# Optimization experiments

Hardware: AMD Instinct MI355X
Metric: run time of the kernel (lower is better)

The kernel has to match this reference:

```python
import jax, jax.numpy as jnp
import numpy as np

L = 16384   # nodes (rows)
E = 131072  # edges
SP = 20000  # column positions (nodes + periodic images)
C = 512     # embed_dim
H = 8       # heads
DH = C // H # head dim = 64
HID = 1024  # ffn hidden


def setup_inputs() -> dict:
    key = jax.random.key(0)
    ks = jax.random.split(key, 16)
    p = lambda k, shape: jax.random.normal(k, shape, dtype=jnp.float32) * 0.02
    return dict(
        x=jax.random.normal(ks[0], (L, C), dtype=jnp.float32),
        row_index=jax.random.randint(ks[1], (E,), 0, L),
        col_index=jax.random.randint(ks[2], (E,), 0, L),
        to_col_index=jax.random.randint(ks[3], (E,), 0, SP),
        att_bias=jax.random.normal(ks[4], (E, H), dtype=jnp.float32),
        pos_att_bias=jax.random.normal(ks[5], (E, H), dtype=jnp.float32),
        dist=jax.random.uniform(ks[6], (E,), minval=0.5, maxval=5.0),
        pos=jax.random.normal(ks[7], (L, 3), dtype=jnp.float32),
        col_pos=jax.random.normal(ks[8], (SP, 3), dtype=jnp.float32),
        ln1_g=jnp.ones((C,), jnp.float32), ln1_b=jnp.zeros((C,), jnp.float32),
        ln2_g=jnp.ones((C,), jnp.float32), ln2_b=jnp.zeros((C,), jnp.float32),
        Wq=p(ks[9], (C, C)), bq=jnp.zeros((C,), jnp.float32),
        Wk=p(ks[10], (C, C)), bk=jnp.zeros((C,), jnp.float32),
        Wv=p(ks[11], (C, C)), bv=jnp.zeros((C,), jnp.float32),
        Wvec=p(ks[12], (3, C)), bvec=jnp.zeros((C,), jnp.float32),
        Wo=p(ks[13], (C, C)), bo=jnp.zeros((C,), jnp.float32),
        W1=p(ks[14], (C, HID)), b1=jnp.zeros((HID,), jnp.float32),
        W2=p(ks[15], (HID, C)), b2=jnp.zeros((C,), jnp.float32),
    )


def _ln(x, g, b, eps=1e-5):
    mu = jnp.mean(x, -1, keepdims=True)
    v = jnp.mean((x - mu) ** 2, -1, keepdims=True)
    return (x - mu) * jax.lax.rsqrt(v + eps) * g + b


def reference(x, row_index, col_index, to_col_index, att_bias, pos_att_bias,
              dist, pos, col_pos, ln1_g, ln1_b, ln2_g, ln2_b,
              Wq, bq, Wk, bk, Wv, bv, Wvec, bvec, Wo, bo, W1, b1, W2, b2):
    Lx = x.shape[0]
    # --- pre-norm + Euclidean sparse attention ---
    z = _ln(x, ln1_g, ln1_b)
    q = (z @ Wq + bq).reshape(Lx, H, DH)
    k = (z @ Wk + bk).reshape(Lx, H, DH)
    v = (z @ Wv + bv).reshape(Lx, H, DH)
    qe = q[row_index]          # (E,H,DH) gather
    ke = k[col_index]          # (E,H,DH)
    ve = v[col_index]          # (E,H,DH)
    # relative unit direction from receiving node to (PBC-shifted) column node
    rel = (col_pos[to_col_index] - pos[row_index]) / dist[:, None]   # (E,3)
    ve = ve + (rel @ Wvec + bvec).reshape(-1, H, DH)
    # Euclidean (negative squared L2) attention score + positional bias
    score = -jnp.sum((qe - ke) ** 2, axis=-1) / np.float32(np.sqrt(DH)) + pos_att_bias  # (E,H)
    # segment softmax over edges grouped by row_index
    m = jax.ops.segment_max(score, row_index, num_segments=Lx)       # (L,H)
    m = jnp.where(jnp.isfinite(m), m, 0.0)
    pexp = jnp.exp(score - m[row_index])
    den = jax.ops.segment_sum(pexp, row_index, num_segments=Lx)      # (L,H)
    deng = den[row_index]
    alpha = pexp / jnp.where(deng == 0.0, 1.0, deng)                 # (E,H)
    out = jax.ops.segment_sum(alpha[:, :, None] * ve, row_index, num_segments=Lx)
    att = out.reshape(Lx, C) @ Wo + bo
    x = x + att
    # --- pre-norm + feed-forward ---
    z2 = _ln(x, ln2_g, ln2_b)
    ff = jax.nn.gelu(z2 @ W1 + b1) @ W2 + b2
    return x + ff
```

## Files before the change

### kernel.cpp

```cpp
#include <hip/hip_runtime.h>

#define L_NODES 16384
#define E_EDGES 131072
#define CDIM 512
#define QKVDIM 1536
#define HEADS 8
#define DHEAD 64
#define HID 1024

typedef __attribute__((ext_vector_type(8))) short bf16x8;
typedef __attribute__((ext_vector_type(4))) float f32x4;

__device__ inline unsigned short f2b(float f) {
    union { float f; unsigned int u; } v{f};
    unsigned int r = (v.u + 0x7fffu + ((v.u >> 16) & 1u)) >> 16;
    return (unsigned short)r;
}
__device__ inline float b2f(unsigned short h) {
    union { unsigned int u; float f; } v;
    v.u = (unsigned int)h << 16;
    return v.f;
}

__device__ inline void async_lds16(const void* g, void* l) {
    __builtin_amdgcn_global_load_lds(
        (const __attribute__((address_space(1))) unsigned int*)g,
        (__attribute__((address_space(3))) unsigned int*)l,
        16, 0, 0);
}

__global__ __launch_bounds__(256) void ln_bf16_kernel(
    const float* __restrict__ x, const float* __restrict__ g,
    const float* __restrict__ b, short* __restrict__ out)
{
    int row = blockIdx.x;
    int t = threadIdx.x;
    const float2* xr = (const float2*)(x + (size_t)row * CDIM);
    float2 v = xr[t];
    float s = v.x + v.y;
    float sq = v.x * v.x + v.y * v.y;
    for (int off = 32; off; off >>= 1) {
        s += __shfl_xor(s, off);
        sq += __shfl_xor(sq, off);
    }
    __shared__ float ss[4], sqs[4];
    int wave = t >> 6, lane = t & 63;
    if (lane == 0) { ss[wave] = s; sqs[wave] = sq; }
    __syncthreads();
    s = ss[0] + ss[1] + ss[2] + ss[3];
    sq = sqs[0] + sqs[1] + sqs[2] + sqs[3];
    float mu = s * (1.0f / CDIM);
    float var = sq * (1.0f / CDIM) - mu * mu;
    float inv = rsqrtf(var + 1e-5f);
    int c = t * 2;
    unsigned short h0 = f2b((v.x - mu) * inv * g[c] + b[c]);
    unsigned short h1 = f2b((v.y - mu) * inv * g[c + 1] + b[c + 1]);
    unsigned int packed = ((unsigned int)h1 << 16) | h0;
    *(unsigned int*)(out + (size_t)row * CDIM + c) = packed;
}

__global__ void transpose_bf16_kernel(const float* __restrict__ W, short* __restrict__ WT,
                                      int K, int N)
{
    __shared__ float tile[32][33];
    int n0 = blockIdx.x * 32, k0 = blockIdx.y * 32;
    int tx = threadIdx.x, ty = threadIdx.y;
    for (int r = 0; r < 4; r++) {
        int k = ty + r * 8;
        tile[k][tx] = W[(size_t)(k0 + k) * N + n0 + tx];
    }
    __syncthreads();
    for (int r = 0; r < 4; r++) {
        int n = ty + r * 8;
        WT[(size_t)(n0 + n) * K + k0 + tx] = f2b(tile[tx][n]);
    }
}

__global__ void pack_bias_kernel(const float* __restrict__ bq, const float* __restrict__ bk,
                                 const float* __restrict__ bv, float* __restrict__ out)
{
    int i = blockIdx.x * 256 + threadIdx.x;
    if (i < CDIM) out[i] = bq[i];
    else if (i < 2 * CDIM) out[i] = bk[i - CDIM];
    else out[i] = bv[i - 2 * CDIM];
}

__global__ __launch_bounds__(256) void gemm_bf16_kernel(
    const short* __restrict__ A, const short* __restrict__ B,
    const float* __restrict__ bias, const float* __restrict__ res,
    float* __restrict__ outf, short* __restrict__ outb,
    int M, int N, int K, int act)
{
    __shared__ short As[128 * 32];
    __shared__ short Bs[128 * 32];
    int t = threadIdx.x;
    int bm = blockIdx.y * 128, bn = blockIdx.x * 128;
    int wave = t >> 6, lane = t & 63;
    int wm = (wave & 1) * 64, wn = (wave >> 1) * 64;
    int crow = lane & 15, quad = lane >> 4;

    f32x4 acc[4][4] = {};

    for (int k0 = 0; k0 < K; k0 += 32) {
#pragma unroll
        for (int c = 0; c < 2; c++) {
            int idx = c * 256 + t;
            int row = idx >> 2, chunk = idx & 3;
            async_lds16(A + (size_t)(bm + row) * K + k0 + chunk * 8,
                        (char*)As + c * 4096 + wave * 1024 + lane * 16);
            async_lds16(B + (size_t)(bn + row) * K + k0 + chunk * 8,
                        (char*)Bs + c * 4096 + wave * 1024 + lane * 16);
        }
        __syncthreads();
        bf16x8 af[4], bg[4];
#pragma unroll
        for (int i = 0; i < 4; i++)
            af[i] = *(const bf16x8*)&As[(wm + i * 16 + crow) * 32 + quad * 8];
#pragma unroll
        for (int j = 0; j < 4; j++)
            bg[j] = *(const bf16x8*)&Bs[(wn + j * 16 + crow) * 32 + quad * 8];
#pragma unroll
        for (int i = 0; i < 4; i++)
#pragma unroll
            for (int j = 0; j < 4; j++)
                acc[i][j] = __builtin_amdgcn_mfma_f32_16x16x32_bf16(af[i], bg[j], acc[i][j], 0, 0, 0);
        __syncthreads();
    }

#pragma unroll
    for (int i = 0; i < 4; i++) {
#pragma unroll
        for (int j = 0; j < 4; j++) {
            int n = bn + wn + j * 16 + crow;
            float bi = bias ? bias[n] : 0.0f;
#pragma unroll
            for (int r = 0; r < 4; r++) {
                int mrow = bm + wm + i * 16 + quad * 4 + r;
                float val = acc[i][j][r] + bi;
                if (act) {
                    float u = 0.7978845608028654f * (val + 0.044715f * val * val * val);
                    val = 0.5f * val * (1.0f + tanhf(u));
                }
                if (res) val += res[(size_t)mrow * N + n];
                if (outf) outf[(size_t)mrow * N + n] = val;
                if (outb) outb[(size_t)mrow * N + n] = f2b(val);
            }
        }
    }
}

__global__ void hist_kernel(const int* __restrict__ row_index, int* __restrict__ cnt)
{
    int e = blockIdx.x * 256 + threadIdx.x;
    if (e < E_EDGES) atomicAdd(&cnt[row_index[e]], 1);
}

__global__ void scan_kernel(const int* __restrict__ cnt, int* __restrict__ row_start,
                            int* __restrict__ cursor)
{
    int t = threadIdx.x;
    const int PER = L_NODES / 64;
    int local = 0;
    for (int i = 0; i < PER; i++) local += cnt[t * PER + i];
    int v = local;
    for (int off = 1; off < 64; off <<= 1) {
        int u = __shfl_up(v, off);
        if (t >= off) v += u;
    }
    int run = v - local;
    for (int i = 0; i < PER; i++) {
        row_start[t * PER + i] = run;
        cursor[t * PER + i] = run;
        run += cnt[t * PER + i];
    }
    if (t == 63) row_start[L_NODES] = run;
}

__global__ void scatter_kernel(const int* __restrict__ row_index, const int* __restrict__ col_index,
                               const int* __restrict__ to_col_index, const float* __restrict__ dist,
                               int* __restrict__ cursor, int4* __restrict__ epack)
{
    int e = blockIdx.x * 256 + threadIdx.x;
    if (e < E_EDGES) {
        int p = atomicAdd(&cursor[row_index[e]], 1);
        epack[p] = make_int4(col_index[e], to_col_index[e], __float_as_int(dist[e]), e);
    }
}

__global__ __launch_bounds__(512) void attn_kernel(
    const short* __restrict__ qkv,
    const int4* __restrict__ epack,
    const float* __restrict__ pos_att_bias,
    const float* __restrict__ pos, const float* __restrict__ col_pos,
    const float* __restrict__ Wvec, const float* __restrict__ bvec,
    const int* __restrict__ row_start,
    short* __restrict__ out_bf)
{
    int r = blockIdx.x;
    int t = threadIdx.x;
    int h = t >> 6;
    int c = t;
    float qv = b2f(((const unsigned short*)qkv)[(size_t)r * QKVDIM + c]);
    float wv0 = Wvec[c], wv1 = Wvec[CDIM + c], wv2 = Wvec[2 * CDIM + c];
    float bv = bvec[c];
    float p0 = pos[r * 3], p1 = pos[r * 3 + 1], p2 = pos[r * 3 + 2];
    int e0 = row_start[r], e1 = row_start[r + 1];
    float m = -1e30f, l = 0.0f, acc = 0.0f;
    const unsigned short* kvbase = (const unsigned short*)qkv;

    int idx = e0;
    for (; idx + 1 < e1; idx += 2) {
        int4 ea = epack[idx], eb = epack[idx + 1];
        size_t ba = (size_t)ea.x * QKVDIM + CDIM + c;
        size_t bb = (size_t)eb.x * QKVDIM + CDIM + c;
        float ka = b2f(kvbase[ba]);
        float va = b2f(kvbase[ba + CDIM]);
        float kb = b2f(kvbase[bb]);
        float vb = b2f(kvbase[bb + CDIM]);
        float biasa = pos_att_bias[ea.w * HEADS + h];
        float biasb = pos_att_bias[eb.w * HEADS + h];
        float dia = 1.0f / __int_as_float(ea.z);
        float dib = 1.0f / __int_as_float(eb.z);
        float ra0 = (col_pos[ea.y * 3] - p0) * dia;
        float ra1 = (col_pos[ea.y * 3 + 1] - p1) * dia;
        float ra2 = (col_pos[ea.y * 3 + 2] - p2) * dia;
        float rb0 = (col_pos[eb.y * 3] - p0) * dib;
        float rb1 = (col_pos[eb.y * 3 + 1] - p1) * dib;
        float rb2 = (col_pos[eb.y * 3 + 2] - p2) * dib;
        va += ra0 * wv0 + ra1 * wv1 + ra2 * wv2 + bv;
        vb += rb0 * wv0 + rb1 * wv1 + rb2 * wv2 + bv;
        float da = qv - ka, db = qv - kb;
        float sa = da * da, sb = db * db;
        for (int off = 32; off; off >>= 1) {
            sa += __shfl_xor(sa, off);
            sb += __shfl_xor(sb, off);
        }
        float s0 = -sa * 0.125f + biasa;
        float s1 = -sb * 0.125f + biasb;
        float mn = fmaxf(m, fmaxf(s0, s1));
        float scale = __expf(m - mn);
        float pa = __expf(s0 - mn);
        float pb = __expf(s1 - mn);
        l = l * scale + pa + pb;
        acc = acc * scale + pa * va + pb * vb;
        m = mn;
    }
    if (idx < e1) {
        int4 ea = epack[idx];
        size_t ba = (size_t)ea.x * QKVDIM + CDIM + c;
        float ka = b2f(kvbase[ba]);
        float va = b2f(kvbase[ba + CDIM]);
        float dia = 1.0f / __int_as_float(ea.z);
        float ra0 = (col_pos[ea.y * 3] - p0) * dia;
        float ra1 = (col_pos[ea.y * 3 + 1] - p1) * dia;
        float ra2 = (col_pos[ea.y * 3 + 2] - p2) * dia;
        va += ra0 * wv0 + ra1 * wv1 + ra2 * wv2 + bv;
        float da = qv - ka;
        float sa = da * da;
        for (int off = 32; off; off >>= 1) sa += __shfl_xor(sa, off);
        float s0 = -sa * 0.125f + pos_att_bias[ea.w * HEADS + h];
        float mn = fmaxf(m, s0);
        float scale = __expf(m - mn);
        float pa = __expf(s0 - mn);
        l = l * scale + pa;
        acc = acc * scale + pa * va;
        m = mn;
    }
    float o = (l > 0.0f) ? acc / l : 0.0f;
    out_bf[(size_t)r * CDIM + c] = f2b(o);
}

extern "C" void kernel_launch(void* const* d_in, const int* in_sizes, int n_in,
                              void* d_out, int out_size, void* d_ws, size_t ws_size,
                              hipStream_t stream)
{
    const float* x            = (const float*)d_in[0];
    const int*   row_index    = (const int*)d_in[1];
    const int*   col_index    = (const int*)d_in[2];
    const int*   to_col_index = (const int*)d_in[3];
    const float* pos_att_bias = (const float*)d_in[5];
    const float* dist         = (const float*)d_in[6];
    const float* pos          = (const float*)d_in[7];
    const float* col_pos      = (const float*)d_in[8];
    const float* ln1_g = (const float*)d_in[9];
    const float* ln1_b = (const float*)d_in[10];
    const float* ln2_g = (const float*)d_in[11];
    const float* ln2_b = (const float*)d_in[12];
    const float* Wq = (const float*)d_in[13];  const float* bq = (const float*)d_in[14];
    const float* Wk = (const float*)d_in[15];  const float* bk = (const float*)d_in[16];
    const float* Wv = (const float*)d_in[17];  const float* bv = (const float*)d_in[18];
    const float* Wvec = (const float*)d_in[19]; const float* bvec = (const float*)d_in[20];
    const float* Wo = (const float*)d_in[21];  const float* bo = (const float*)d_in[22];
    const float* W1 = (const float*)d_in[23];  const float* b1 = (const float*)d_in[24];
    const float* W2 = (const float*)d_in[25];  const float* b2 = (const float*)d_in[26];

    char* ws = (char*)d_ws;
    size_t off = 0;
    auto alloc = [&](size_t bytes) -> void* {
        void* p = ws + off;
        off = (off + bytes + 255) & ~(size_t)255;
        return p;
    };
    const size_t LC = (size_t)L_NODES * CDIM;
    short* qkvb = (short*)alloc((size_t)L_NODES * QKVDIM * 2);
    float* x1f  = (float*)alloc(LC * 4);
    short* zbf  = (short*)alloc(LC * 2);
    short* abf  = (short*)alloc(LC * 2);
    short* wqkvT = (short*)alloc((size_t)QKVDIM * CDIM * 2);
    short* woT   = (short*)alloc((size_t)CDIM * CDIM * 2);
    short* w1T   = (short*)alloc((size_t)CDIM * HID * 2);
    short* w2T   = (short*)alloc((size_t)HID * CDIM * 2);
    float* bqkv  = (float*)alloc(QKVDIM * 4);
    int* cnt       = (int*)alloc(L_NODES * 4);
    int* cursor    = (int*)alloc(L_NODES * 4);
    int* row_start = (int*)alloc((L_NODES + 1) * 4);
    int4* epack    = (int4*)alloc((size_t)E_EDGES * 16);
    short* hbf = (short*)qkvb;

    hipMemsetAsync(cnt, 0, L_NODES * 4, stream);

    dim3 tb(32, 8);
    transpose_bf16_kernel<<<dim3(CDIM / 32, CDIM / 32), tb, 0, stream>>>(Wq, wqkvT, CDIM, CDIM);
    transpose_bf16_kernel<<<dim3(CDIM / 32, CDIM / 32), tb, 0, stream>>>(Wk, wqkvT + (size_t)CDIM * CDIM, CDIM, CDIM);
    transpose_bf16_kernel<<<dim3(CDIM / 32, CDIM / 32), tb, 0, stream>>>(Wv, wqkvT + (size_t)2 * CDIM * CDIM, CDIM, CDIM);
    transpose_bf16_kernel<<<dim3(CDIM / 32, CDIM / 32), tb, 0, stream>>>(Wo, woT, CDIM, CDIM);
    transpose_bf16_kernel<<<dim3(HID / 32, CDIM / 32), tb, 0, stream>>>(W1, w1T, CDIM, HID);
    transpose_bf16_kernel<<<dim3(CDIM / 32, HID / 32), tb, 0, stream>>>(W2, w2T, HID, CDIM);
    pack_bias_kernel<<<QKVDIM / 256, 256, 0, stream>>>(bq, bk, bv, bqkv);

    ln_bf16_kernel<<<L_NODES, 256, 0, stream>>>(x, ln1_g, ln1_b, zbf);

    dim3 gqkv(QKVDIM / 128, L_NODES / 128);
    gemm_bf16_kernel<<<gqkv, 256, 0, stream>>>(zbf, wqkvT, bqkv, nullptr, nullptr, qkvb,
                                               L_NODES, QKVDIM, CDIM, 0);

    hist_kernel<<<E_EDGES / 256, 256, 0, stream>>>(row_index, cnt);
    scan_kernel<<<1, 64, 0, stream>>>(cnt, row_start, cursor);
    scatter_kernel<<<E_EDGES / 256, 256, 0, stream>>>(row_index, col_index, to_col_index, dist,
                                                      cursor, epack);

    attn_kernel<<<L_NODES, 512, 0, stream>>>(qkvb, epack, pos_att_bias, pos, col_pos,
                                             Wvec, bvec, row_start, abf);

    dim3 g512(CDIM / 128, L_NODES / 128);
    gemm_bf16_kernel<<<g512, 256, 0, stream>>>(abf, woT, bo, x, x1f, nullptr, L_NODES, CDIM, CDIM, 0);

    ln_bf16_kernel<<<L_NODES, 256, 0, stream>>>(x1f, ln2_g, ln2_b, zbf);

    dim3 g1024(HID / 128, L_NODES / 128);
    gemm_bf16_kernel<<<g1024, 256, 0, stream>>>(zbf, w1T, b1, nullptr, nullptr, hbf, L_NODES, HID, CDIM, 1);
    gemm_bf16_kernel<<<g512, 256, 0, stream>>>(hbf, w2T, b2, x1f, (float*)d_out, nullptr, L_NODES, CDIM, HID, 0);
}
```

Baseline: 497.0 us.

## Process 8 edges per wave in attention, precompute edge geometry, fuse prep kernels

The attention kernel now assigns each wave one head, with 8 lanes per edge and 8 channels per lane. This gives 16-byte vectorized K/V loads and 8 edges in flight per iteration, in place of 2-byte scalar loads on 2 edges. The scatter step now precomputes the relative direction vector and permutes pos_att_bias into CSR order, reusing the x1f buffer, so the attention loop drops the col_pos/pos gathers and the divide. The weight transposes, bias packing and counter memset are merged into one prep kernel to cut launch count. The cost is more registers per thread and a cross-lane reduction at the end.

```diff
diff --git a/kernel.cpp b/kernel.cpp
--- a/kernel.cpp
+++ b/kernel.cpp
@@ -59,30 +59,52 @@
     *(unsigned int*)(out + (size_t)row * CDIM + c) = packed;
 }
 
-__global__ void transpose_bf16_kernel(const float* __restrict__ W, short* __restrict__ WT,
-                                      int K, int N)
-{
+__global__ __launch_bounds__(256) void prep_kernel(
+    const float* __restrict__ Wq, const float* __restrict__ Wk,
+    const float* __restrict__ Wv, const float* __restrict__ Wo,
+    const float* __restrict__ W1, const float* __restrict__ W2,
+    short* __restrict__ wqkvT, short* __restrict__ woT,
+    short* __restrict__ w1T, short* __restrict__ w2T,
+    const float* __restrict__ bq, const float* __restrict__ bk,
+    const float* __restrict__ bv, float* __restrict__ bqkv,
+    int* __restrict__ cnt)
+{
+    int bid = blockIdx.x;
+    if (bid >= 2054) {
+        cnt[(bid - 2054) * 256 + threadIdx.x] = 0;
+        return;
+    }
+    if (bid >= 2048) {
+        int i = (bid - 2048) * 256 + threadIdx.x;
+        float val = (i < CDIM) ? bq[i] : (i < 2 * CDIM) ? bk[i - CDIM] : bv[i - 2 * CDIM];
+        bqkv[i] = val;
+        return;
+    }
+    const float* W; short* WT; int K, N, tn, tk;
+    if (bid < 1024) {
+        int w = bid >> 8, local = bid & 255;
+        tn = local & 15; tk = local >> 4; K = 512; N = 512;
+        W = (w == 0) ? Wq : (w == 1) ? Wk : (w == 2) ? Wv : Wo;
+        WT = (w == 3) ? woT : wqkvT + (size_t)w * 512 * 512;
+    } else if (bid < 1536) {
+        int local = bid - 1024;
+        tn = local & 31; tk = local >> 5; K = 512; N = 1024;
+        W = W1; WT = w1T;
+    } else {
+        int local = bid - 1536;
+        tn = local & 15; tk = local >> 4; K = 1024; N = 512;
+        W = W2; WT = w2T;
+    }
     __shared__ float tile[32][33];
-    int n0 = blockIdx.x * 32, k0 = blockIdx.y * 32;
-    int tx = threadIdx.x, ty = threadIdx.y;
-    for (int r = 0; r < 4; r++) {
-        int k = ty + r * 8;
-        tile[k][tx] = W[(size_t)(k0 + k) * N + n0 + tx];
-    }
+    int tx = threadIdx.x & 31, ty = threadIdx.x >> 5;
+    int n0 = tn * 32, k0 = tk * 32;
+#pragma unroll
+    for (int r = 0; r < 4; r++)
+        tile[ty + r * 8][tx] = W[(size_t)(k0 + ty + r * 8) * N + n0 + tx];
     __syncthreads();
-    for (int r = 0; r < 4; r++) {
-        int n = ty + r * 8;
-        WT[(size_t)(n0 + n) * K + k0 + tx] = f2b(tile[tx][n]);
-    }
-}
-
-__global__ void pack_bias_kernel(const float* __restrict__ bq, const float* __restrict__ bk,
-                                 const float* __restrict__ bv, float* __restrict__ out)
-{
-    int i = blockIdx.x * 256 + threadIdx.x;
-    if (i < CDIM) out[i] = bq[i];
-    else if (i < 2 * CDIM) out[i] = bk[i - CDIM];
-    else out[i] = bv[i - 2 * CDIM];
+#pragma unroll
+    for (int r = 0; r < 4; r++)
+        WT[(size_t)(n0 + ty + r * 8) * K + k0 + tx] = f2b(tile[tx][ty + r * 8]);
 }
 
 __global__ __launch_bounds__(256) void gemm_bf16_kernel(
@@ -178,96 +200,116 @@
 
 __global__ void scatter_kernel(const int* __restrict__ row_index, const int* __restrict__ col_index,
                                const int* __restrict__ to_col_index, const float* __restrict__ dist,
-                               int* __restrict__ cursor, int4* __restrict__ epack)
+                               const float* __restrict__ pos, const float* __restrict__ col_pos,
+                               const float* __restrict__ pos_att_bias,
+                               int* __restrict__ cursor, int4* __restrict__ emeta,
+                               float* __restrict__ pabp)
 {
     int e = blockIdx.x * 256 + threadIdx.x;
     if (e < E_EDGES) {
-        int p = atomicAdd(&cursor[row_index[e]], 1);
-        epack[p] = make_int4(col_index[e], to_col_index[e], __float_as_int(dist[e]), e);
+        int row = row_index[e];
+        int p = atomicAdd(&cursor[row], 1);
+        int tci = to_col_index[e];
+        float dinv = 1.0f / dist[e];
+        float r0 = (col_pos[tci * 3]     - pos[row * 3])     * dinv;
+        float r1 = (col_pos[tci * 3 + 1] - pos[row * 3 + 1]) * dinv;
+        float r2 = (col_pos[tci * 3 + 2] - pos[row * 3 + 2]) * dinv;
+        emeta[p] = make_int4(col_index[e], __float_as_int(r0), __float_as_int(r1),
+                             __float_as_int(r2));
+        const float4* pb = (const float4*)(pos_att_bias + (size_t)e * HEADS);
+        float4 b0 = pb[0], b1 = pb[1];
+        float4* dst = (float4*)(pabp + (size_t)p * HEADS);
+        dst[0] = b0; dst[1] = b1;
     }
 }
 
 __global__ __launch_bounds__(512) void attn_kernel(
-    const short* __restrict__ qkv,
-    const int4* __restrict__ epack,
-    const float* __restrict__ pos_att_bias,
-    const float* __restrict__ pos, const float* __restrict__ col_pos,
+    const short* __restrict__ qkv, const int4* __restrict__ emeta,
+    const float* __restrict__ pabp, const int* __restrict__ row_start,
     const float* __restrict__ Wvec, const float* __restrict__ bvec,
-    const int* __restrict__ row_start,
     short* __restrict__ out_bf)
 {
     int r = blockIdx.x;
     int t = threadIdx.x;
-    int h = t >> 6;
-    int c = t;
-    float qv = b2f(((const unsigned short*)qkv)[(size_t)r * QKVDIM + c]);
-    float wv0 = Wvec[c], wv1 = Wvec[CDIM + c], wv2 = Wvec[2 * CDIM + c];
-    float bv = bvec[c];
-    float p0 = pos[r * 3], p1 = pos[r * 3 + 1], p2 = pos[r * 3 + 2];
+    int h = t >> 6, lane = t & 63;
+    int es = lane >> 3, ch = lane & 7;
+    int cbase = h * DHEAD + ch * 8;
+
+    float qv[8], wv0[8], wv1[8], wv2[8], bvv[8];
+    {
+        bf16x8 qh = *(const bf16x8*)(qkv + (size_t)r * QKVDIM + cbase);
+#pragma unroll
+        for (int j = 0; j < 8; j++) qv[j] = b2f((unsigned short)qh[j]);
+        float4 a0 = *(const float4*)(Wvec + cbase);
+        float4 a1 = *(const float4*)(Wvec + cbase + 4);
+        float4 b0 = *(const float4*)(Wvec + CDIM + cbase);
+        float4 b1 = *(const float4*)(Wvec + CDIM + cbase + 4);
+        float4 c0 = *(const float4*)(Wvec + 2 * CDIM + cbase);
+        float4 c1 = *(const float4*)(Wvec + 2 * CDIM + cbase + 4);
+        float4 d0 = *(const float4*)(bvec + cbase);
+        float4 d1 = *(const float4*)(bvec + cbase + 4);
+        wv0[0]=a0.x; wv0[1]=a0.y; wv0[2]=a0.z; wv0[3]=a0.w; wv0[4]=a1.x; wv0[5]=a1.y; wv0[6]=a1.z; wv0[7]=a1.w;
+        wv1[0]=b0.x; wv1[1]=b0.y; wv1[2]=b0.z; wv1[3]=b0.w; wv1[4]=b1.x; wv1[5]=b1.y; wv1[6]=b1.z; wv1[7]=b1.w;
+        wv2[0]=c0.x; wv2[1]=c0.y; wv2[2]=c0.z; wv2[3]=c0.w; wv2[4]=c1.x; wv2[5]=c1.y; wv2[6]=c1.z; wv2[7]=c1.w;
+        bvv[0]=d0.x; bvv[1]=d0.y; bvv[2]=d0.z; bvv[3]=d0.w; bvv[4]=d1.x; bvv[5]=d1.y; bvv[6]=d1.z; bvv[7]=d1.w;
+    }
+
     int e0 = row_start[r], e1 = row_start[r + 1];
-    float m = -1e30f, l = 0.0f, acc = 0.0f;
-    const unsigned short* kvbase = (const unsigned short*)qkv;
-
-    int idx = e0;
-    for (; idx + 1 < e1; idx += 2) {
-        int4 ea = epack[idx], eb = epack[idx + 1];
-        size_t ba = (size_t)ea.x * QKVDIM + CDIM + c;
-        size_t bb = (size_t)eb.x * QKVDIM + CDIM + c;
-        float ka = b2f(kvbase[ba]);
-        float va = b2f(kvbase[ba + CDIM]);
-        float kb = b2f(kvbase[bb]);
-        float vb = b2f(kvbase[bb + CDIM]);
-        float biasa = pos_att_bias[ea.w * HEADS + h];
-        float biasb = pos_att_bias[eb.w * HEADS + h];
-        float dia = 1.0f / __int_as_float(ea.z);
-        float dib = 1.0f / __int_as_float(eb.z);
-        float ra0 = (col_pos[ea.y * 3] - p0) * dia;
-        float ra1 = (col_pos[ea.y * 3 + 1] - p1) * dia;
-        float ra2 = (col_pos[ea.y * 3 + 2] - p2) * dia;
-        float rb0 = (col_pos[eb.y * 3] - p0) * dib;
-        float rb1 = (col_pos[eb.y * 3 + 1] - p1) * dib;
-        float rb2 = (col_pos[eb.y * 3 + 2] - p2) * dib;
-        va += ra0 * wv0 + ra1 * wv1 + ra2 * wv2 + bv;
-        vb += rb0 * wv0 + rb1 * wv1 + rb2 * wv2 + bv;
-        float da = qv - ka, db = qv - kb;
-        float sa = da * da, sb = db * db;
-        for (int off = 32; off; off >>= 1) {
-            sa += __shfl_xor(sa, off);
-            sb += __shfl_xor(sb, off);
+    float m = -1e30f, l = 0.0f;
+    float acc[8] = {};
+
+    for (int idx = e0; idx < e1; idx += 8) {
+        int myidx = idx + es;
+        bool act = myidx < e1;
+        int cidx = act ? myidx : (e1 - 1);
+        int4 em = emeta[cidx];
+        float pab = pabp[(size_t)cidx * HEADS + h];
+        const short* kp = qkv + (size_t)em.x * QKVDIM + CDIM + cbase;
+        bf16x8 k8 = *(const bf16x8*)kp;
+        bf16x8 v8 = *(const bf16x8*)(kp + CDIM);
+        float s = 0.0f;
+        float vf[8];
+#pragma unroll
+        for (int j = 0; j < 8; j++) {
+            float kf = b2f((unsigned short)k8[j]);
+            vf[j] = b2f((unsigned short)v8[j]);
+            float d = qv[j] - kf;
+            s = fmaf(d, d, s);
         }
-        float s0 = -sa * 0.125f + biasa;
-        float s1 = -sb * 0.125f + biasb;
-        float mn = fmaxf(m, fmaxf(s0, s1));
+        s += __shfl_xor(s, 1);
+        s += __shfl_xor(s, 2);
+        s += __shfl_xor(s, 4);
+        float score = act ? (-s * 0.125f + pab) : -1e30f;
+        float bmax = score;
+        bmax = fmaxf(bmax, __shfl_xor(bmax, 8));
+        bmax = fmaxf(bmax, __shfl_xor(bmax, 16));
+        bmax = fmaxf(bmax, __shfl_xor(bmax, 32));
+        float mn = fmaxf(m, bmax);
         float scale = __expf(m - mn);
-        float pa = __expf(s0 - mn);
-        float pb = __expf(s1 - mn);
-        l = l * scale + pa + pb;
-        acc = acc * scale + pa * va + pb * vb;
+        float pexp = __expf(score - mn);
         m = mn;
-    }
-    if (idx < e1) {
-        int4 ea = epack[idx];
-        size_t ba = (size_t)ea.x * QKVDIM + CDIM + c;
-        float ka = b2f(kvbase[ba]);
-        float va = b2f(kvbase[ba + CDIM]);
-        float dia = 1.0f / __int_as_float(ea.z);
-        float ra0 = (col_pos[ea.y * 3] - p0) * dia;
-        float ra1 = (col_pos[ea.y * 3 + 1] - p1) * dia;
-        float ra2 = (col_pos[ea.y * 3 + 2] - p2) * dia;
-        va += ra0 * wv0 + ra1 * wv1 + ra2 * wv2 + bv;
-        float da = qv - ka;
-        float sa = da * da;
-        for (int off = 32; off; off >>= 1) sa += __shfl_xor(sa, off);
-        float s0 = -sa * 0.125f + pos_att_bias[ea.w * HEADS + h];
-        float mn = fmaxf(m, s0);
-        float scale = __expf(m - mn);
-        float pa = __expf(s0 - mn);
-        l = l * scale + pa;
-        acc = acc * scale + pa * va;
-        m = mn;
-    }
-    float o = (l > 0.0f) ? acc / l : 0.0f;
-    out_bf[(size_t)r * CDIM + c] = f2b(o);
+        l = l * scale + pexp;
+        float r0 = __int_as_float(em.y), r1 = __int_as_float(em.z), r2 = __int_as_float(em.w);
+#pragma unroll
+        for (int j = 0; j < 8; j++) {
+            float vv = vf[j] + r0 * wv0[j] + r1 * wv1[j] + r2 * wv2[j] + bvv[j];
+            acc[j] = acc[j] * scale + pexp * vv;
+        }
+    }
+    l += __shfl_xor(l, 8); l += __shfl_xor(l, 16); l += __shfl_xor(l, 32);
+#pragma unroll
+    for (int j = 0; j < 8; j++) {
+        acc[j] += __shfl_xor(acc[j], 8);
+        acc[j] += __shfl_xor(acc[j], 16);
+        acc[j] += __shfl_xor(acc[j], 32);
+    }
+    float inv = (l > 0.0f) ? 1.0f / l : 0.0f;
+    if (es == 0) {
+        bf16x8 o;
+#pragma unroll
+        for (int j = 0; j < 8; j++) o[j] = (short)f2b(acc[j] * inv);
+        *(bf16x8*)(out_bf + (size_t)r * CDIM + cbase) = o;
+    }
 }
 
 extern "C" void kernel_launch(void* const* d_in, const int* in_sizes, int n_in,
@@ -314,19 +356,13 @@
     int* cnt       = (int*)alloc(L_NODES * 4);
     int* cursor    = (int*)alloc(L_NODES * 4);
     int* row_start = (int*)alloc((L_NODES + 1) * 4);
-    int4* epack    = (int4*)alloc((size_t)E_EDGES * 16);
+    int4* emeta    = (int4*)alloc((size_t)E_EDGES * 16);
     short* hbf = (short*)qkvb;
-
-    hipMemsetAsync(cnt, 0, L_NODES * 4, stream);
-
-    dim3 tb(32, 8);
-    transpose_bf16_kernel<<<dim3(CDIM / 32, CDIM / 32), tb, 0, stream>>>(Wq, wqkvT, CDIM, CDIM);
-    transpose_bf16_kernel<<<dim3(CDIM / 32, CDIM / 32), tb, 0, stream>>>(Wk, wqkvT + (size_t)CDIM * CDIM, CDIM, CDIM);
-    transpose_bf16_kernel<<<dim3(CDIM / 32, CDIM / 32), tb, 0, stream>>>(Wv, wqkvT + (size_t)2 * CDIM * CDIM, CDIM, CDIM);
-    transpose_bf16_kernel<<<dim3(CDIM / 32, CDIM / 32), tb, 0, stream>>>(Wo, woT, CDIM, CDIM);
-    transpose_bf16_kernel<<<dim3(HID / 32, CDIM / 32), tb, 0, stream>>>(W1, w1T, CDIM, HID);
-    transpose_bf16_kernel<<<dim3(CDIM / 32, HID / 32), tb, 0, stream>>>(W2, w2T, HID, CDIM);
-    pack_bias_kernel<<<QKVDIM / 256, 256, 0, stream>>>(bq, bk, bv, bqkv);
+    float* pabp = x1f;
+
+    prep_kernel<<<2118, 256, 0, stream>>>(Wq, Wk, Wv, Wo, W1, W2,
+                                          wqkvT, woT, w1T, w2T,
+                                          bq, bk, bv, bqkv, cnt);
 
     ln_bf16_kernel<<<L_NODES, 256, 0, stream>>>(x, ln1_g, ln1_b, zbf);
 
@@ -336,11 +372,11 @@
 
     hist_kernel<<<E_EDGES / 256, 256, 0, stream>>>(row_index, cnt);
     scan_kernel<<<1, 64, 0, stream>>>(cnt, row_start, cursor);
-    scatter_kernel<<<E_EDGES / 256, 256, 0, stream>>>(row_index, col_index, to_col_index, dist,
-                                                      cursor, epack);
-
-    attn_kernel<<<L_NODES, 512, 0, stream>>>(qkvb, epack, pos_att_bias, pos, col_pos,
-                                             Wvec, bvec, row_start, abf);
+    scatter_kernel<<<E_EDGES / 256, 256, 0, stream>>>(row_index, col_index, to_col_index,
+                                                      dist, pos, col_pos, pos_att_bias,
+                                                      cursor, emeta, pabp);
+
+    attn_kernel<<<L_NODES, 512, 0, stream>>>(qkvb, emeta, pabp, row_start, Wvec, bvec, abf);
 
     dim3 g512(CDIM / 128, L_NODES / 128);
     gemm_bf16_kernel<<<g512, 256, 0, stream>>>(abf, woT, bo, x, x1f, nullptr, L_NODES, CDIM, CDIM, 0);
```

Result: slower. 507.2 us (+2.1%).
